# Kernel tuning notes

Measured on AMD Instinct MI355X. Metric: run time of the kernel, lower is better.

## Reference

```python
import jax, jax.numpy as jnp
import numpy as np
import math

EMB = 768
HEADS = 12
HEAD_DIM = EMB // HEADS
FF = 3072
EPS = 1e-5


def setup_inputs() -> dict:
    key = jax.random.key(0)
    ks = jax.random.split(key, 12)
    s = 0.02
    return {
        "x": jax.random.normal(ks[0], (8, 1024, EMB), dtype=jnp.float32),
        "qkv_w": jax.random.normal(ks[1], (EMB, 3 * EMB), dtype=jnp.float32) * s,
        "qkv_b": jnp.zeros((3 * EMB,), dtype=jnp.float32),
        "out_w": jax.random.normal(ks[2], (EMB, EMB), dtype=jnp.float32) * s,
        "out_b": jnp.zeros((EMB,), dtype=jnp.float32),
        "ln1_g": jnp.ones((EMB,), dtype=jnp.float32),
        "ln1_b": jnp.zeros((EMB,), dtype=jnp.float32),
        "ln2_g": jnp.ones((EMB,), dtype=jnp.float32),
        "ln2_b": jnp.zeros((EMB,), dtype=jnp.float32),
        "fc1_w": jax.random.normal(ks[3], (EMB, FF), dtype=jnp.float32) * s,
        "fc1_b": jnp.zeros((FF,), dtype=jnp.float32),
        "fc2_w": jax.random.normal(ks[4], (FF, EMB), dtype=jnp.float32) * s,
        "fc2_b": jnp.zeros((EMB,), dtype=jnp.float32),
    }


def layernorm(x, g, b):
    mu = jnp.mean(x, axis=-1, keepdims=True)
    var = jnp.var(x, axis=-1, keepdims=True)
    return (x - mu) * jax.lax.rsqrt(var + EPS) * g + b


def new_gelu(x):
    c = math.sqrt(2.0 / math.pi)
    return 0.5 * x * (1.0 + jnp.tanh(c * (x + 0.044715 * x * x * x)))


def reference(x, qkv_w, qkv_b, out_w, out_b, ln1_g, ln1_b, ln2_g, ln2_b,
              fc1_w, fc1_b, fc2_w, fc2_b):
    B, S, _ = x.shape
    # --- attention sublayer (pre-LN) ---
    h = layernorm(x, ln1_g, ln1_b)
    qkv = h @ qkv_w + qkv_b                      # [B,S,3E]
    q, k, v = jnp.split(qkv, 3, axis=-1)
    def heads(t):
        return t.reshape(B, S, HEADS, HEAD_DIM).transpose(0, 2, 1, 3)  # [B,H,S,D]
    q, k, v = heads(q), heads(k), heads(v)
    scores = jnp.einsum('bhsd,bhtd->bhst', q, k) / math.sqrt(HEAD_DIM)
    probs = jax.nn.softmax(scores, axis=-1)
    attn = jnp.einsum('bhst,bhtd->bhsd', probs, v)
    attn = attn.transpose(0, 2, 1, 3).reshape(B, S, EMB)
    attn = attn @ out_w + out_b
    x = x + attn
    # --- MLP sublayer (pre-LN) ---
    h = layernorm(x, ln2_g, ln2_b)
    h = new_gelu(h @ fc1_w + fc1_b)
    h = h @ fc2_w + fc2_b
    return x + h
```

## Files before the change

kernel.cpp:

```cpp
#include <hip/hip_runtime.h>

typedef __bf16 bf16x8 __attribute__((ext_vector_type(8)));
typedef __bf16 bf16x2 __attribute__((ext_vector_type(2)));
typedef float  f32x4  __attribute__((ext_vector_type(4)));

#define EMB 768
#define HEADS 12
#define HD 64
#define FF 3072
#define SEQ 1024
#define BATCH 8
#define ROWS (BATCH*SEQ)
#define QKVSZ ((size_t)BATCH*HEADS*SEQ*HD)

__global__ __launch_bounds__(256) void ln_kernel(const float* __restrict__ x,
        const float* __restrict__ g, const float* __restrict__ b,
        __bf16* __restrict__ out)
{
    int row = blockIdx.x;
    int tid = threadIdx.x;
    const float* xr = x + (size_t)row * EMB;
    float v0 = xr[tid], v1 = xr[tid + 256], v2 = xr[tid + 512];
    float s  = v0 + v1 + v2;
    float ss = v0*v0 + v1*v1 + v2*v2;
    #pragma unroll
    for (int off = 32; off >= 1; off >>= 1) {
        s  += __shfl_xor(s, off);
        ss += __shfl_xor(ss, off);
    }
    __shared__ float red[2][4];
    int wave = tid >> 6;
    if ((tid & 63) == 0) { red[0][wave] = s; red[1][wave] = ss; }
    __syncthreads();
    s  = red[0][0] + red[0][1] + red[0][2] + red[0][3];
    ss = red[1][0] + red[1][1] + red[1][2] + red[1][3];
    float mu  = s * (1.0f / EMB);
    float var = ss * (1.0f / EMB) - mu * mu;
    float inv = rsqrtf(var + 1e-5f);
    __bf16* orow = out + (size_t)row * EMB;
    orow[tid]       = (__bf16)((v0 - mu) * inv * g[tid]       + b[tid]);
    orow[tid + 256] = (__bf16)((v1 - mu) * inv * g[tid + 256] + b[tid + 256]);
    orow[tid + 512] = (__bf16)((v2 - mu) * inv * g[tid + 512] + b[tid + 512]);
}

__global__ __launch_bounds__(256) void transpose_convert(const float* __restrict__ W,
        __bf16* __restrict__ WT, int K, int N)
{
    __shared__ float t[32][33];
    int nb = blockIdx.x * 32, kb = blockIdx.y * 32;
    int tx = threadIdx.x, ty = threadIdx.y;
    #pragma unroll
    for (int i = 0; i < 32; i += 8)
        t[ty + i][tx] = W[(size_t)(kb + ty + i) * N + nb + tx];
    __syncthreads();
    #pragma unroll
    for (int i = 0; i < 32; i += 8)
        WT[(size_t)(nb + ty + i) * K + kb + tx] = (__bf16)t[tx][ty + i];
}

template<int EPI>
__global__ __launch_bounds__(256) void gemm_bt(
    const __bf16* __restrict__ A, const __bf16* __restrict__ BT,
    const float* __restrict__ bias, const float* __restrict__ resid,
    void* __restrict__ outp, int M, int N, int K)
{
    __shared__ __bf16 Al[128][40];
    __shared__ __bf16 Bl[128][40];
    int tid  = threadIdx.x;
    int lane = tid & 63, wave = tid >> 6;
    int wr = wave >> 1, wc = wave & 1;
    int lr = lane & 15, lg = lane >> 4;
    int bn = blockIdx.x * 128, bm = blockIdx.y * 128;
    int r0 = tid >> 2, c0 = (tid & 3) * 8;
    const __bf16* Ap = A  + (size_t)(bm + r0) * K + c0;
    const __bf16* Bp = BT + (size_t)(bn + r0) * K + c0;

    f32x4 acc[4][4];
    #pragma unroll
    for (int i = 0; i < 4; i++)
        #pragma unroll
        for (int j = 0; j < 4; j++) acc[i][j] = (f32x4){0.f, 0.f, 0.f, 0.f};

    for (int k0 = 0; k0 < K; k0 += 32) {
        int4 a0 = *(const int4*)(Ap + k0);
        int4 a1 = *(const int4*)(Ap + (size_t)64 * K + k0);
        int4 b0 = *(const int4*)(Bp + k0);
        int4 b1 = *(const int4*)(Bp + (size_t)64 * K + k0);
        __syncthreads();
        *(int4*)&Al[r0][c0]      = a0;
        *(int4*)&Al[r0 + 64][c0] = a1;
        *(int4*)&Bl[r0][c0]      = b0;
        *(int4*)&Bl[r0 + 64][c0] = b1;
        __syncthreads();
        bf16x8 af[4], bfr[4];
        #pragma unroll
        for (int mi = 0; mi < 4; mi++) af[mi]  = *(const bf16x8*)&Al[wr*64 + mi*16 + lr][lg*8];
        #pragma unroll
        for (int ni = 0; ni < 4; ni++) bfr[ni] = *(const bf16x8*)&Bl[wc*64 + ni*16 + lr][lg*8];
        #pragma unroll
        for (int mi = 0; mi < 4; mi++)
            #pragma unroll
            for (int ni = 0; ni < 4; ni++)
                acc[mi][ni] = __builtin_amdgcn_mfma_f32_16x16x32_bf16(af[mi], bfr[ni], acc[mi][ni], 0, 0, 0);
    }

    #pragma unroll
    for (int mi = 0; mi < 4; mi++) {
        int row = bm + wr*64 + mi*16 + lg*4;
        #pragma unroll
        for (int ni = 0; ni < 4; ni++) {
            int col = bn + wc*64 + ni*16 + lr;
            float bv = bias[col];
            #pragma unroll
            for (int j = 0; j < 4; j++) {
                int r = row + j;
                float v = acc[mi][ni][j] + bv;
                if (EPI == 0) {
                    int which = col / 768;
                    int cc = col - which * 768;
                    int hh = cc >> 6, dd = cc & 63;
                    int bb = r >> 10, s = r & 1023;
                    if (which == 0) v *= 0.125f;
                    ((__bf16*)outp)[(size_t)which * QKVSZ +
                        ((((size_t)bb * HEADS + hh) << 10) + s) * HD + dd] = (__bf16)v;
                } else if (EPI == 1) {
                    ((float*)outp)[(size_t)r * N + col] = v + resid[(size_t)r * N + col];
                } else {
                    float u = 0.7978845608028654f * (v + 0.044715f * v * v * v);
                    float e = __expf(2.0f * u);
                    float th = 1.0f - 2.0f / (e + 1.0f);
                    ((__bf16*)outp)[(size_t)r * N + col] = (__bf16)(0.5f * v * (1.0f + th));
                }
            }
        }
    }
}

__global__ __launch_bounds__(256) void attn_kernel(
    const __bf16* __restrict__ Q, const __bf16* __restrict__ Km,
    const __bf16* __restrict__ V, __bf16* __restrict__ Aout)
{
    int blk = blockIdx.x;
    int bh = blk >> 4, qt = blk & 15;
    int bb = bh / HEADS, hh = bh % HEADS;
    const __bf16* Qp = Q  + (size_t)bh * SEQ * HD;
    const __bf16* Kp = Km + (size_t)bh * SEQ * HD;
    const __bf16* Vp = V  + (size_t)bh * SEQ * HD;
    int tid = threadIdx.x;
    int lane = tid & 63, wave = tid >> 6;
    int lr = lane & 15, lg = lane >> 4;

    __shared__ __bf16 P[4][16][72];
    __shared__ __bf16 Vt[64][72];

    int qrow = qt * 64 + wave * 16 + lr;
    bf16x8 qf[2];
    #pragma unroll
    for (int ks = 0; ks < 2; ks++)
        qf[ks] = *(const bf16x8*)(Qp + (size_t)qrow * HD + ks * 32 + lg * 8);

    f32x4 o[4];
    #pragma unroll
    for (int i = 0; i < 4; i++) o[i] = (f32x4){0.f, 0.f, 0.f, 0.f};
    float m = -1e30f, l = 0.0f;

    for (int t = 0; t < 16; ++t) {
        f32x4 st[4];
        #pragma unroll
        for (int i = 0; i < 4; i++) st[i] = (f32x4){0.f, 0.f, 0.f, 0.f};
        #pragma unroll
        for (int ks = 0; ks < 2; ks++)
            #pragma unroll
            for (int mf = 0; mf < 4; mf++) {
                bf16x8 kf = *(const bf16x8*)(Kp + (size_t)(t*64 + mf*16 + lr) * HD + ks*32 + lg*8);
                st[mf] = __builtin_amdgcn_mfma_f32_16x16x32_bf16(kf, qf[ks], st[mf], 0, 0, 0);
            }

        __syncthreads();
        {
            int kk = tid >> 3;
            int d0 = (tid & 7) * 8;
            #pragma unroll
            for (int rep = 0; rep < 2; ++rep) {
                bf16x8 vv = *(const bf16x8*)(Vp + (size_t)(t*64 + kk + rep*32) * HD + d0);
                #pragma unroll
                for (int i = 0; i < 8; i++) Vt[d0 + i][kk + rep*32] = vv[i];
            }
        }
        float pmax = -1e30f;
        #pragma unroll
        for (int mf = 0; mf < 4; mf++)
            #pragma unroll
            for (int j = 0; j < 4; j++) pmax = fmaxf(pmax, st[mf][j]);
        pmax = fmaxf(pmax, __shfl_xor(pmax, 16));
        pmax = fmaxf(pmax, __shfl_xor(pmax, 32));
        float mn = fmaxf(m, pmax);
        float scale = __expf(m - mn);
        float ps = 0.0f;
        #pragma unroll
        for (int mf = 0; mf < 4; mf++) {
            float p0 = __expf(st[mf][0] - mn), p1 = __expf(st[mf][1] - mn);
            float p2 = __expf(st[mf][2] - mn), p3 = __expf(st[mf][3] - mn);
            ps += (p0 + p1) + (p2 + p3);
            bf16x2 w01 = {(__bf16)p0, (__bf16)p1};
            bf16x2 w23 = {(__bf16)p2, (__bf16)p3};
            *(bf16x2*)&P[wave][lr][mf*16 + lg*4]     = w01;
            *(bf16x2*)&P[wave][lr][mf*16 + lg*4 + 2] = w23;
        }
        ps += __shfl_xor(ps, 16);
        ps += __shfl_xor(ps, 32);
        l = l * scale + ps;
        m = mn;
        __syncthreads();

        float sc0 = __shfl(scale, lg*4 + 0), sc1 = __shfl(scale, lg*4 + 1);
        float sc2 = __shfl(scale, lg*4 + 2), sc3 = __shfl(scale, lg*4 + 3);
        #pragma unroll
        for (int nf = 0; nf < 4; nf++) {
            o[nf][0] *= sc0; o[nf][1] *= sc1; o[nf][2] *= sc2; o[nf][3] *= sc3;
        }
        #pragma unroll
        for (int ks = 0; ks < 2; ks++) {
            bf16x8 pf = *(const bf16x8*)&P[wave][lr][ks*32 + lg*8];
            #pragma unroll
            for (int nf = 0; nf < 4; nf++) {
                bf16x8 vf = *(const bf16x8*)&Vt[nf*16 + lr][ks*32 + lg*8];
                o[nf] = __builtin_amdgcn_mfma_f32_16x16x32_bf16(pf, vf, o[nf], 0, 0, 0);
            }
        }
    }

    float l0 = __shfl(l, lg*4 + 0), l1 = __shfl(l, lg*4 + 1);
    float l2 = __shfl(l, lg*4 + 2), l3 = __shfl(l, lg*4 + 3);
    f32x4 linv = {1.0f/l0, 1.0f/l1, 1.0f/l2, 1.0f/l3};
    #pragma unroll
    for (int nf = 0; nf < 4; nf++) {
        int d = nf*16 + lr;
        #pragma unroll
        for (int j = 0; j < 4; j++) {
            int q = qt*64 + wave*16 + lg*4 + j;
            Aout[((size_t)bb * SEQ + q) * EMB + hh * HD + d] = (__bf16)(o[nf][j] * linv[j]);
        }
    }
}

extern "C" void kernel_launch(void* const* d_in, const int* in_sizes, int n_in,
                              void* d_out, int out_size, void* d_ws, size_t ws_size,
                              hipStream_t stream) {
    const float* x      = (const float*)d_in[0];
    const float* qkv_w  = (const float*)d_in[1];
    const float* qkv_b  = (const float*)d_in[2];
    const float* out_w  = (const float*)d_in[3];
    const float* out_b  = (const float*)d_in[4];
    const float* ln1_g  = (const float*)d_in[5];
    const float* ln1_b  = (const float*)d_in[6];
    const float* ln2_g  = (const float*)d_in[7];
    const float* ln2_b  = (const float*)d_in[8];
    const float* fc1_w  = (const float*)d_in[9];
    const float* fc1_b  = (const float*)d_in[10];
    const float* fc2_w  = (const float*)d_in[11];
    const float* fc2_b  = (const float*)d_in[12];

    char* ws = (char*)d_ws;
    __bf16* wqkvT  = (__bf16*)(ws + 0);
    __bf16* woutT  = (__bf16*)(ws + 3538944);
    __bf16* wfc1T  = (__bf16*)(ws + 4718592);
    __bf16* wfc2T  = (__bf16*)(ws + 9437184);
    float*  x1     = (float*) (ws + 14155776);
    __bf16* hbuf   = (__bf16*)(ws + 39321600);
    __bf16* qbuf   = (__bf16*)(ws + 51904512);
    __bf16* attn   = (__bf16*)(ws + 89653248);
    __bf16* fc1out = (__bf16*)(ws + 51904512);

    transpose_convert<<<dim3(2304/32, 768/32),  dim3(32,8), 0, stream>>>(qkv_w, wqkvT, 768, 2304);
    transpose_convert<<<dim3(768/32,  768/32),  dim3(32,8), 0, stream>>>(out_w, woutT, 768, 768);
    transpose_convert<<<dim3(3072/32, 768/32),  dim3(32,8), 0, stream>>>(fc1_w, wfc1T, 768, 3072);
    transpose_convert<<<dim3(768/32,  3072/32), dim3(32,8), 0, stream>>>(fc2_w, wfc2T, 3072, 768);

    ln_kernel<<<ROWS, 256, 0, stream>>>(x, ln1_g, ln1_b, hbuf);
    gemm_bt<0><<<dim3(2304/128, ROWS/128), 256, 0, stream>>>(hbuf, wqkvT, qkv_b, nullptr, qbuf, ROWS, 2304, 768);
    attn_kernel<<<BATCH*HEADS*(SEQ/64), 256, 0, stream>>>(qbuf, qbuf + QKVSZ, qbuf + 2*QKVSZ, attn);
    gemm_bt<1><<<dim3(768/128, ROWS/128), 256, 0, stream>>>(attn, woutT, out_b, x, x1, ROWS, 768, 768);
    ln_kernel<<<ROWS, 256, 0, stream>>>(x1, ln2_g, ln2_b, hbuf);
    gemm_bt<2><<<dim3(3072/128, ROWS/128), 256, 0, stream>>>(hbuf, wfc1T, fc1_b, nullptr, fc1out, ROWS, 3072, 768);
    gemm_bt<1><<<dim3(768/128, ROWS/128), 256, 0, stream>>>(fc1out, wfc2T, fc2_b, x1, (float*)d_out, ROWS, 768, 3072);
}
```

Baseline: 492.0 us.

## Use direct global-to-LDS loads in GEMM and pre-transpose V for attention

The GEMM now stages A/B tiles with global_load_lds (16-byte direct-to-LDS) and drops the LDS row padding. That avoids the register round trip but may add bank conflicts, and it adds a trailing barrier. V is transposed once into a separate buffer by a new kernel, so the attention loop reads V fragments straight from global memory instead of transposing into shared memory each tile. This removes two block barriers per iteration in attention. P stores are widened to 4-element vectors.

Result: slower. 533.0 us (+8.4%).

```diff
diff --git a/kernel.cpp b/kernel.cpp
--- a/kernel.cpp
+++ b/kernel.cpp
@@ -1,7 +1,7 @@
 #include <hip/hip_runtime.h>
 
 typedef __bf16 bf16x8 __attribute__((ext_vector_type(8)));
-typedef __bf16 bf16x2 __attribute__((ext_vector_type(2)));
+typedef __bf16 bf16x4 __attribute__((ext_vector_type(4)));
 typedef float  f32x4  __attribute__((ext_vector_type(4)));
 
 #define EMB 768
@@ -12,6 +12,13 @@
 #define BATCH 8
 #define ROWS (BATCH*SEQ)
 #define QKVSZ ((size_t)BATCH*HEADS*SEQ*HD)
+
+__device__ __forceinline__ void gload16(const void* g, void* l) {
+    __builtin_amdgcn_global_load_lds(
+        (const __attribute__((address_space(1))) unsigned int*)g,
+        (__attribute__((address_space(3))) unsigned int*)l,
+        16, 0, 0);
+}
 
 __global__ __launch_bounds__(256) void ln_kernel(const float* __restrict__ x,
         const float* __restrict__ g, const float* __restrict__ b,
@@ -58,22 +65,52 @@
         WT[(size_t)(nb + ty + i) * K + kb + tx] = (__bf16)t[tx][ty + i];
 }
 
+__global__ __launch_bounds__(256) void vtrans_kernel(const __bf16* __restrict__ V,
+        __bf16* __restrict__ Vt)
+{
+    __shared__ __bf16 t[64][72];
+    int bh = blockIdx.x >> 4, st = blockIdx.x & 15;
+    const __bf16* Vp = V + ((size_t)bh * SEQ + st * 64) * HD;
+    int r  = threadIdx.x >> 3;
+    int c0 = (threadIdx.x & 7) * 8;
+    #pragma unroll
+    for (int rep = 0; rep < 2; rep++)
+        *(bf16x8*)&t[r + rep*32][c0] = *(const bf16x8*)(Vp + (size_t)(r + rep*32) * HD + c0);
+    __syncthreads();
+    #pragma unroll
+    for (int rep = 0; rep < 2; rep++) {
+        int dd = r + rep*32;
+        bf16x8 o;
+        #pragma unroll
+        for (int j = 0; j < 8; j++) o[j] = t[c0 + j][dd];
+        *(bf16x8*)(Vt + ((size_t)bh * HD + dd) * SEQ + st * 64 + c0) = o;
+    }
+}
+
 template<int EPI>
 __global__ __launch_bounds__(256) void gemm_bt(
     const __bf16* __restrict__ A, const __bf16* __restrict__ BT,
     const float* __restrict__ bias, const float* __restrict__ resid,
     void* __restrict__ outp, int M, int N, int K)
 {
-    __shared__ __bf16 Al[128][40];
-    __shared__ __bf16 Bl[128][40];
+    __shared__ __bf16 Al[128][32];
+    __shared__ __bf16 Bl[128][32];
     int tid  = threadIdx.x;
     int lane = tid & 63, wave = tid >> 6;
     int wr = wave >> 1, wc = wave & 1;
     int lr = lane & 15, lg = lane >> 4;
     int bn = blockIdx.x * 128, bm = blockIdx.y * 128;
-    int r0 = tid >> 2, c0 = (tid & 3) * 8;
-    const __bf16* Ap = A  + (size_t)(bm + r0) * K + c0;
-    const __bf16* Bp = BT + (size_t)(bn + r0) * K + c0;
+
+    int srow = wave * 16 + (lane >> 2);
+    int scol = (lane & 3) * 8;
+    const __bf16* Ag0 = A  + (size_t)(bm + srow) * K + scol;
+    const __bf16* Ag1 = Ag0 + (size_t)64 * K;
+    const __bf16* Bg0 = BT + (size_t)(bn + srow) * K + scol;
+    const __bf16* Bg1 = Bg0 + (size_t)64 * K;
+    __bf16* lA0 = &Al[wave * 16][0];
+    __bf16* lA1 = &Al[64 + wave * 16][0];
+    __bf16* lB0 = &Bl[wave * 16][0];
+    __bf16* lB1 = &Bl[64 + wave * 16][0];
 
     f32x4 acc[4][4];
     #pragma unroll
@@ -82,15 +119,10 @@
         for (int j = 0; j < 4; j++) acc[i][j] = (f32x4){0.f, 0.f, 0.f, 0.f};
 
     for (int k0 = 0; k0 < K; k0 += 32) {
-        int4 a0 = *(const int4*)(Ap + k0);
-        int4 a1 = *(const int4*)(Ap + (size_t)64 * K + k0);
-        int4 b0 = *(const int4*)(Bp + k0);
-        int4 b1 = *(const int4*)(Bp + (size_t)64 * K + k0);
-        __syncthreads();
-        *(int4*)&Al[r0][c0]      = a0;
-        *(int4*)&Al[r0 + 64][c0] = a1;
-        *(int4*)&Bl[r0][c0]      = b0;
-        *(int4*)&Bl[r0 + 64][c0] = b1;
+        gload16(Ag0 + k0, lA0);
+        gload16(Ag1 + k0, lA1);
+        gload16(Bg0 + k0, lB0);
+        gload16(Bg1 + k0, lB1);
         __syncthreads();
         bf16x8 af[4], bfr[4];
         #pragma unroll
@@ -102,6 +134,7 @@
             #pragma unroll
             for (int ni = 0; ni < 4; ni++)
                 acc[mi][ni] = __builtin_amdgcn_mfma_f32_16x16x32_bf16(af[mi], bfr[ni], acc[mi][ni], 0, 0, 0);
+        __syncthreads();
     }
 
     #pragma unroll
@@ -138,20 +171,19 @@
 
 __global__ __launch_bounds__(256) void attn_kernel(
     const __bf16* __restrict__ Q, const __bf16* __restrict__ Km,
-    const __bf16* __restrict__ V, __bf16* __restrict__ Aout)
+    const __bf16* __restrict__ Vt, __bf16* __restrict__ Aout)
 {
     int blk = blockIdx.x;
     int bh = blk >> 4, qt = blk & 15;
     int bb = bh / HEADS, hh = bh % HEADS;
     const __bf16* Qp = Q  + (size_t)bh * SEQ * HD;
     const __bf16* Kp = Km + (size_t)bh * SEQ * HD;
-    const __bf16* Vp = V  + (size_t)bh * SEQ * HD;
+    const __bf16* Vp = Vt + (size_t)bh * SEQ * HD;
     int tid = threadIdx.x;
     int lane = tid & 63, wave = tid >> 6;
     int lr = lane & 15, lg = lane >> 4;
 
     __shared__ __bf16 P[4][16][72];
-    __shared__ __bf16 Vt[64][72];
 
     int qrow = qt * 64 + wave * 16 + lr;
     bf16x8 qf[2];
@@ -165,33 +197,22 @@
     float m = -1e30f, l = 0.0f;
 
     for (int t = 0; t < 16; ++t) {
-        f32x4 st[4];
-        #pragma unroll
-        for (int i = 0; i < 4; i++) st[i] = (f32x4){0.f, 0.f, 0.f, 0.f};
+        f32x4 st4[4];
+        #pragma unroll
+        for (int i = 0; i < 4; i++) st4[i] = (f32x4){0.f, 0.f, 0.f, 0.f};
         #pragma unroll
         for (int ks = 0; ks < 2; ks++)
             #pragma unroll
             for (int mf = 0; mf < 4; mf++) {
                 bf16x8 kf = *(const bf16x8*)(Kp + (size_t)(t*64 + mf*16 + lr) * HD + ks*32 + lg*8);
-                st[mf] = __builtin_amdgcn_mfma_f32_16x16x32_bf16(kf, qf[ks], st[mf], 0, 0, 0);
+                st4[mf] = __builtin_amdgcn_mfma_f32_16x16x32_bf16(kf, qf[ks], st4[mf], 0, 0, 0);
             }
 
-        __syncthreads();
-        {
-            int kk = tid >> 3;
-            int d0 = (tid & 7) * 8;
-            #pragma unroll
-            for (int rep = 0; rep < 2; ++rep) {
-                bf16x8 vv = *(const bf16x8*)(Vp + (size_t)(t*64 + kk + rep*32) * HD + d0);
-                #pragma unroll
-                for (int i = 0; i < 8; i++) Vt[d0 + i][kk + rep*32] = vv[i];
-            }
-        }
         float pmax = -1e30f;
         #pragma unroll
         for (int mf = 0; mf < 4; mf++)
             #pragma unroll
-            for (int j = 0; j < 4; j++) pmax = fmaxf(pmax, st[mf][j]);
+            for (int j = 0; j < 4; j++) pmax = fmaxf(pmax, st4[mf][j]);
         pmax = fmaxf(pmax, __shfl_xor(pmax, 16));
         pmax = fmaxf(pmax, __shfl_xor(pmax, 32));
         float mn = fmaxf(m, pmax);
@@ -199,19 +220,16 @@
         float ps = 0.0f;
         #pragma unroll
         for (int mf = 0; mf < 4; mf++) {
-            float p0 = __expf(st[mf][0] - mn), p1 = __expf(st[mf][1] - mn);
-            float p2 = __expf(st[mf][2] - mn), p3 = __expf(st[mf][3] - mn);
+            float p0 = __expf(st4[mf][0] - mn), p1 = __expf(st4[mf][1] - mn);
+            float p2 = __expf(st4[mf][2] - mn), p3 = __expf(st4[mf][3] - mn);
             ps += (p0 + p1) + (p2 + p3);
-            bf16x2 w01 = {(__bf16)p0, (__bf16)p1};
-            bf16x2 w23 = {(__bf16)p2, (__bf16)p3};
-            *(bf16x2*)&P[wave][lr][mf*16 + lg*4]     = w01;
-            *(bf16x2*)&P[wave][lr][mf*16 + lg*4 + 2] = w23;
+            bf16x4 w = {(__bf16)p0, (__bf16)p1, (__bf16)p2, (__bf16)p3};
+            *(bf16x4*)&P[wave][lr][mf*16 + lg*4] = w;
         }
         ps += __shfl_xor(ps, 16);
         ps += __shfl_xor(ps, 32);
         l = l * scale + ps;
         m = mn;
-        __syncthreads();
 
         float sc0 = __shfl(scale, lg*4 + 0), sc1 = __shfl(scale, lg*4 + 1);
         float sc2 = __shfl(scale, lg*4 + 2), sc3 = __shfl(scale, lg*4 + 3);
@@ -224,7 +242,7 @@
             bf16x8 pf = *(const bf16x8*)&P[wave][lr][ks*32 + lg*8];
             #pragma unroll
             for (int nf = 0; nf < 4; nf++) {
-                bf16x8 vf = *(const bf16x8*)&Vt[nf*16 + lr][ks*32 + lg*8];
+                bf16x8 vf = *(const bf16x8*)(Vp + (size_t)(nf*16 + lr) * SEQ + t*64 + ks*32 + lg*8);
                 o[nf] = __builtin_amdgcn_mfma_f32_16x16x32_bf16(pf, vf, o[nf], 0, 0, 0);
             }
         }
@@ -271,6 +289,7 @@
     __bf16* qbuf   = (__bf16*)(ws + 51904512);
     __bf16* attn   = (__bf16*)(ws + 89653248);
     __bf16* fc1out = (__bf16*)(ws + 51904512);
+    __bf16* vt     = hbuf;
 
     transpose_convert<<<dim3(2304/32, 768/32),  dim3(32,8), 0, stream>>>(qkv_w, wqkvT, 768, 2304);
     transpose_convert<<<dim3(768/32,  768/32),  dim3(32,8), 0, stream>>>(out_w, woutT, 768, 768);
@@ -279,7 +298,8 @@
 
     ln_kernel<<<ROWS, 256, 0, stream>>>(x, ln1_g, ln1_b, hbuf);
     gemm_bt<0><<<dim3(2304/128, ROWS/128), 256, 0, stream>>>(hbuf, wqkvT, qkv_b, nullptr, qbuf, ROWS, 2304, 768);
-    attn_kernel<<<BATCH*HEADS*(SEQ/64), 256, 0, stream>>>(qbuf, qbuf + QKVSZ, qbuf + 2*QKVSZ, attn);
+    vtrans_kernel<<<BATCH*HEADS*(SEQ/64), 256, 0, stream>>>(qbuf + 2*QKVSZ, vt);
+    attn_kernel<<<BATCH*HEADS*(SEQ/64), 256, 0, stream>>>(qbuf, qbuf + QKVSZ, vt, attn);
     gemm_bt<1><<<dim3(768/128, ROWS/128), 256, 0, stream>>>(attn, woutT, out_b, x, x1, ROWS, 768, 768);
     ln_kernel<<<ROWS, 256, 0, stream>>>(x1, ln2_g, ln2_b, hbuf);
     gemm_bt<2><<<dim3(3072/128, ROWS/128), 256, 0, stream>>>(hbuf, wfc1T, fc1_b, nullptr, fc1out, ROWS, 3072, 768);
```
